# Kernel tuning notes

Hardware: AMD Instinct MI355X
Metric: run time of the kernel (lower is better)

Reference implementation:

```python
import jax, jax.numpy as jnp
import numpy as np

N_NODES = 100000

def gcn_conv(x, edge_index, W, b, n_nodes):
    # GCNConv: out = D^{-1/2} (A + I) D^{-1/2} X W + b  (self-loops added)
    src, dst = edge_index[0], edge_index[1]
    loops = jnp.arange(n_nodes, dtype=edge_index.dtype)
    src = jnp.concatenate([src, loops])
    dst = jnp.concatenate([dst, loops])
    deg = jax.ops.segment_sum(jnp.ones_like(dst, dtype=x.dtype), dst, num_segments=n_nodes)
    dinv = jnp.where(deg > 0, jax.lax.rsqrt(deg), 0.0)
    norm = dinv[src] * dinv[dst]  # [E+N]
    h = x @ W  # transform first (small d), then gather/scatter
    msgs = h[src] * norm[:, None]
    out = jax.ops.segment_sum(msgs, dst, num_segments=n_nodes)
    return out + b


def setup_inputs() -> dict:
    key = jax.random.key(0)
    k1, k2, k3, k4, k5, k6 = jax.random.split(key, 6)
    x = jax.random.normal(k1, (N_NODES, 3), dtype=jnp.float32)
    edge_index = jax.random.randint(k2, (2, 2400000), 0, N_NODES, dtype=jnp.int64)
    # Glorot-style init for GCNConv linear weights; zero bias matches PyG default
    W1 = jax.random.normal(k3, (3, 16), dtype=jnp.float32) * (1.0 / np.sqrt(3))
    b1 = jnp.zeros((16,), dtype=jnp.float32)
    W2 = jax.random.normal(k4, (16, 32), dtype=jnp.float32) * (1.0 / np.sqrt(16))
    b2 = jnp.zeros((32,), dtype=jnp.float32)
    return {"x": x, "edge_index": edge_index, "W1": W1, "b1": b1, "W2": W2, "b2": b2}


def reference(x, edge_index, W1, b1, W2, b2):
    n = x.shape[0]
    h = gcn_conv(x, edge_index, W1, b1, n)
    h = jax.nn.relu(h)
    h = gcn_conv(h, edge_index, W2, b2, n)
    # batch is all zeros in the original forward -> single-graph mean pool
    return jnp.mean(h, axis=0, keepdims=True)  # [1, 32]
```

## Files before the change

### kernel.cpp

```cpp
#include <hip/hip_runtime.h>

typedef unsigned int uint;
typedef unsigned long long ull;
typedef unsigned char uchar;


#define MAXB  256
#define CAP   16384u
#define BINB  512
#define CHUNK 4096
#define AFS   2048.0f
#define AFB   16384
#define AFM   0x1FFFFFu
#define PADN  131072

__global__ void __launch_bounds__(BINB)
bin2_kernel(const int* __restrict__ srcI, const int* __restrict__ dstI,
            uint* __restrict__ curDg, uint* __restrict__ curSg,
            uint* __restrict__ bufD, uint* __restrict__ bufS, int E) {
    __shared__ uint cntD[MAXB], scanD[MAXB], deltaD[MAXB];
    __shared__ uint cntS[MAXB], scanS[MAXB], deltaS[MAXB];
    __shared__ uint stageD[CHUNK];
    __shared__ uint stageS[CHUNK];
    __shared__ uchar stBD[CHUNK];
    __shared__ uchar stBS[CHUNK];
    const int tid = threadIdx.x;
    const int e0 = blockIdx.x * CHUNK;
    const int nE = min(CHUNK, E - e0);
    const int my0 = tid * 8;
    const int myc = max(0, min(8, nE - my0));
    if (tid < MAXB) cntD[tid] = 0u; else cntS[tid - MAXB] = 0u;

    uint d8[8], s8[8], rD[8], rS[8];
    if (myc == 8) {
        int4 ka = ((const int4*)(dstI + e0))[tid * 2];
        int4 kb = ((const int4*)(dstI + e0))[tid * 2 + 1];
        int4 oa = ((const int4*)(srcI + e0))[tid * 2];
        int4 ob = ((const int4*)(srcI + e0))[tid * 2 + 1];
        d8[0] = ka.x; d8[1] = ka.y; d8[2] = ka.z; d8[3] = ka.w;
        d8[4] = kb.x; d8[5] = kb.y; d8[6] = kb.z; d8[7] = kb.w;
        s8[0] = oa.x; s8[1] = oa.y; s8[2] = oa.z; s8[3] = oa.w;
        s8[4] = ob.x; s8[5] = ob.y; s8[6] = ob.z; s8[7] = ob.w;
    } else {
        for (int r = 0; r < myc; ++r) {
            d8[r] = (uint)dstI[e0 + my0 + r];
            s8[r] = (uint)srcI[e0 + my0 + r];
        }
    }
    __syncthreads();
    for (int r = 0; r < myc; ++r) {
        rD[r] = atomicAdd(&cntD[d8[r] >> 9], 1u);
        rS[r] = atomicAdd(&cntS[s8[r] >> 9], 1u);
    }
    __syncthreads();
    {
        const int wv = tid >> 6, lane = tid & 63;
        if (wv < 2) {
            uint* cn = wv ? cntS : cntD;
            uint* sc = wv ? scanS : scanD;
            uint v0 = cn[lane * 4], v1 = cn[lane * 4 + 1],
                 v2 = cn[lane * 4 + 2], v3 = cn[lane * 4 + 3];
            uint s1 = v0 + v1, s2 = s1 + v2, s3 = s2 + v3;
            uint tot = s3;
            for (int off = 1; off < 64; off <<= 1) {
                uint t = __shfl_up(tot, off, 64);
                if (lane >= off) tot += t;
            }
            uint basex = tot - s3;
            sc[lane * 4]     = basex + v0;
            sc[lane * 4 + 1] = basex + s1;
            sc[lane * 4 + 2] = basex + s2;
            sc[lane * 4 + 3] = basex + s3;
        }
    }
    __syncthreads();
    {
        const int half = tid >> 8;
        const int li = tid & 255;
        uint* cn = half ? cntS : cntD;
        uint* sc = half ? scanS : scanD;
        uint* cur = half ? curSg : curDg;
        uint* dl = half ? deltaS : deltaD;
        uint gbase = (uint)li * CAP + (cn[li] ? atomicAdd(&cur[li * 16], cn[li]) : 0u);
        dl[li] = gbase - (sc[li] - cn[li]);
    }
    __syncthreads();
    for (int r = 0; r < myc; ++r) {
        uint bD = d8[r] >> 9;
        uint pD = (scanD[bD] - cntD[bD]) + rD[r];
        stageD[pD] = ((d8[r] & 511u) << 17) | s8[r];
        stBD[pD] = (uchar)bD;
        uint bS = s8[r] >> 9;
        uint pS = (scanS[bS] - cntS[bS]) + rS[r];
        stageS[pS] = ((s8[r] & 511u) << 17) | d8[r];
        stBS[pS] = (uchar)bS;
    }
    __syncthreads();
#pragma unroll
    for (int r = 0; r < 8; ++r) {
        int i = r * BINB + tid;
        if (i < nE) {
            uint b = stBD[i];
            uint gp = deltaD[b] + (uint)i;
            if (gp < (b + 1u) * CAP) bufD[gp] = stageD[i];
            uint b2 = stBS[i];
            uint gp2 = deltaS[b2] + (uint)i;
            if (gp2 < (b2 + 1u) * CAP) bufS[gp2] = stageS[i];
        }
    }
}

__global__ void __launch_bounds__(1024)
degnode_kernel(const uint* __restrict__ buf, const uint* __restrict__ curD,
               const float* __restrict__ x, uint* __restrict__ degg,
               float* __restrict__ dinv, ull* __restrict__ pxd, int n) {
    __shared__ uint dg[512];
    const int tid = threadIdx.x;
    const int b = blockIdx.x;
    const uint base = (uint)b * CAP;
    const uint c = min(curD[b * 16], CAP);
    if (tid < 512) dg[tid] = 0u;
    __syncthreads();
    for (uint i0 = (uint)tid * 8u; i0 < c; i0 += 8192u) {
        uint cnt8 = min(8u, c - i0);
        uint en[8];
        if (cnt8 == 8u) {
            uint4 a = ((const uint4*)(buf + base + i0))[0];
            uint4 bb = ((const uint4*)(buf + base + i0))[1];
            en[0] = a.x; en[1] = a.y; en[2] = a.z; en[3] = a.w;
            en[4] = bb.x; en[5] = bb.y; en[6] = bb.z; en[7] = bb.w;
        } else {
            for (uint r = 0; r < cnt8; ++r) en[r] = buf[base + i0 + r];
        }
        for (uint r = 0; r < cnt8; ++r) atomicAdd(&dg[en[r] >> 17], 1u);
    }
    __syncthreads();
    if (tid < 512) {
        int node = (b << 9) + tid;
        if (node < n) {
            uint d = dg[tid];
            degg[node] = d;
            float di = rsqrtf((float)(d + 1u));
            dinv[node] = di;
            ull f0 = (ull)(uint)((int)rintf(x[3 * node] * di * AFS) + AFB);
            ull f1 = (ull)(uint)((int)rintf(x[3 * node + 1] * di * AFS) + AFB);
            ull f2 = (ull)(uint)((int)rintf(x[3 * node + 2] * di * AFS) + AFB);
            pxd[node] = f0 | (f1 << 21) | (f2 << 42);
        }
    }
}

__global__ void __launch_bounds__(1024)
aggqT_kernel(const uint* __restrict__ bufD, const uint* __restrict__ curD,
             const uint* __restrict__ bufS, const uint* __restrict__ curS,
             const uint* __restrict__ degg, const float* __restrict__ dinv,
             const ull* __restrict__ pxd, const float* __restrict__ x,
             const float* __restrict__ W1, const float* __restrict__ b1,
             const float* __restrict__ W2, const float* __restrict__ b2,
             float* __restrict__ T, uint* __restrict__ doneCtr,
             float* __restrict__ out, int n) {
    __shared__ ull acc[512];
    __shared__ float gl[512];
    __shared__ float taccs[16];
    __shared__ float tval[16];
    __shared__ int lastB;
    const int tid = threadIdx.x;
    const int b = blockIdx.x;
    const uint base = (uint)b * CAP;
    const uint cD = min(curD[b * 16], CAP);
    const uint cS = min(curS[b * 16], CAP);
    if (tid < 512) { acc[tid] = 0ull; gl[tid] = 0.0f; }
    if (tid < 16) taccs[tid] = 0.0f;
    __syncthreads();
    const int sweep = tid >> 9;
    const uint ht = (uint)(tid & 511);
    if (sweep == 0) {
        for (uint i0 = ht * 8u; i0 < cS; i0 += 4096u) {
            uint cnt8 = min(8u, cS - i0);
            uint en[8];
            if (cnt8 == 8u) {
                uint4 a = ((const uint4*)(bufS + base + i0))[0];
                uint4 bb = ((const uint4*)(bufS + base + i0))[1];
                en[0] = a.x; en[1] = a.y; en[2] = a.z; en[3] = a.w;
                en[4] = bb.x; en[5] = bb.y; en[6] = bb.z; en[7] = bb.w;
            } else {
                for (uint r = 0; r < cnt8; ++r) en[r] = bufS[base + i0 + r];
                for (uint r = cnt8; r < 8u; ++r) en[r] = en[0];
            }
            float dv[8];
#pragma unroll
            for (int r = 0; r < 8; ++r) dv[r] = dinv[en[r] & 0x1FFFFu];
#pragma unroll
            for (uint r = 0; r < 8u; ++r)
                if (r < cnt8) atomicAdd(&gl[en[r] >> 17], dv[r]);
        }
    } else {
        for (uint i0 = ht * 8u; i0 < cD; i0 += 4096u) {
            uint cnt8 = min(8u, cD - i0);
            uint en[8];
            if (cnt8 == 8u) {
                uint4 a = ((const uint4*)(bufD + base + i0))[0];
                uint4 bb = ((const uint4*)(bufD + base + i0))[1];
                en[0] = a.x; en[1] = a.y; en[2] = a.z; en[3] = a.w;
                en[4] = bb.x; en[5] = bb.y; en[6] = bb.z; en[7] = bb.w;
            } else {
                for (uint r = 0; r < cnt8; ++r) en[r] = bufD[base + i0 + r];
                for (uint r = cnt8; r < 8u; ++r) en[r] = en[0];
            }
            ull gv[8];
#pragma unroll
            for (int r = 0; r < 8; ++r) gv[r] = pxd[en[r] & 0x1FFFFu];
#pragma unroll
            for (uint r = 0; r < 8u; ++r)
                if (r < cnt8) atomicAdd(&acc[en[r] >> 17], gv[r]);
        }
    }
    __syncthreads();
    float sq[16];
#pragma unroll
    for (int k = 0; k < 16; ++k) sq[k] = 0.0f;
    if (tid < 512) {
        int node = (b << 9) + tid;
        if (node < n) {
            ull v = acc[tid];
            int ub = (int)(degg[node] * (uint)AFB);
            float di = dinv[node];
            const float isc = 1.0f / AFS;
            float av = (float)((int)(uint)(v & AFM) - ub) * isc + x[3 * node] * di;
            float bv = (float)((int)(uint)((v >> 21) & AFM) - ub) * isc + x[3 * node + 1] * di;
            float cv = (float)((int)(uint)((v >> 42) & AFM) - ub) * isc + x[3 * node + 2] * di;
            float w = gl[tid] + di;
#pragma unroll
            for (int k = 0; k < 16; ++k) {
                float h = di * (av * W1[k] + bv * W1[16 + k] + cv * W1[32 + k]) + b1[k];
                h = fmaxf(h, 0.0f);
                sq[k] = w * (di * h);
            }
        }
    }
#pragma unroll
    for (int k = 0; k < 16; ++k) {
        float v2 = sq[k];
        for (int off = 32; off > 0; off >>= 1) v2 += __shfl_down(v2, off, 64);
        if ((tid & 63) == 0) atomicAdd(&taccs[k], v2);
    }
    __syncthreads();
    if (tid < 16 && taccs[tid] != 0.0f) atomicAdd(&T[tid], taccs[tid]);
    __syncthreads();
    if (tid == 0) {
        __threadfence();
        uint t = atomicAdd(doneCtr, 1u);
        lastB = (t == (uint)(gridDim.x - 1)) ? 1 : 0;
    }
    __syncthreads();
    if (lastB) {
        if (tid < 16) tval[tid] = atomicAdd(&T[tid], 0.0f);
        __syncthreads();
        if (tid < 32) {
            float s2 = 0.0f;
#pragma unroll
            for (int k = 0; k < 16; ++k) s2 += tval[k] * W2[k * 32 + tid];
            out[tid] = b2[tid] + (1.0f / (float)n) * s2;
        }
    }
}

extern "C" void kernel_launch(void* const* d_in, const int* in_sizes, int n_in,
                              void* d_out, int out_size, void* d_ws, size_t ws_size,
                              hipStream_t stream) {
    const float* x   = (const float*)d_in[0];
    const int*   ei  = (const int*)d_in[1];
    const float* W1  = (const float*)d_in[2];
    const float* b1  = (const float*)d_in[3];
    const float* W2  = (const float*)d_in[4];
    const float* b2  = (const float*)d_in[5];
    float* out = (float*)d_out;

    const int n = in_sizes[0] / 3;
    const int E = in_sizes[1] / 2;
    const int* src = ei;
    const int* dst = ei + E;

    char* p = (char*)d_ws;
    float* T    = (float*)p;    p += 64;
    uint*  done = (uint*)p;     p += 64;
    uint*  curD = (uint*)p;     p += MAXB * 16 * 4;
    uint*  curS = (uint*)p;     p += MAXB * 16 * 4;
    size_t zbytes = (size_t)(p - (char*)d_ws);
    uint*  degg  = (uint*)p;    p += (size_t)n * 4;
    float* dinv  = (float*)p;   p += (size_t)n * 4;
    uint*  bufD  = (uint*)p;    p += (size_t)MAXB * CAP * 4;
    uint*  bufS  = (uint*)p;    p += (size_t)MAXB * CAP * 4;
    p = (char*)(((size_t)p + 31) & ~(size_t)31);
    ull*   pxd   = (ull*)p;     p += (size_t)PADN * 8;

    const int nb = (n + 511) >> 9;

    hipMemsetAsync(d_ws, 0, zbytes, stream);
    bin2_kernel<<<(E + CHUNK - 1) / CHUNK, BINB, 0, stream>>>(src, dst, curD, curS, bufD, bufS, E);
    degnode_kernel<<<nb, 1024, 0, stream>>>(bufD, curD, x, degg, dinv, pxd, n);
    aggqT_kernel<<<nb, 1024, 0, stream>>>(bufD, curD, bufS, curS, degg, dinv, pxd, x,
                                          W1, b1, W2, b2, T, done, out, n);
}
```

Before: 136.4 us.

## Fuse degree and aggregation kernels with an in-kernel grid barrier

Merges the degree-counting and node-prep kernel into the aggregation kernel. A software global barrier (atomic counter plus spin-wait) separates the phase that writes pxd/dinv from the gather phase. Each block keeps its own degree histogram in shared memory, so the degg array and one kernel launch gap go away. With 196 blocks of 1024 threads, all blocks must be co-resident or the barrier deadlocks; the guard counter only bounds the spin.

Measured after the change: 149.0 us. 1.09x slower.

```diff
diff --git a/kernel.cpp b/kernel.cpp
--- a/kernel.cpp
+++ b/kernel.cpp
@@ -110,55 +110,31 @@
     }
 }
 
+__device__ __forceinline__ void gbar(uint* ctr, uint target) {
+    __syncthreads();
+    if (threadIdx.x == 0) {
+        __threadfence();
+        atomicAdd(ctr, 1u);
+        uint guard = 0u;
+        while (__hip_atomic_load(ctr, __ATOMIC_ACQUIRE,
+                                 __HIP_MEMORY_SCOPE_AGENT) < target) {
+            __builtin_amdgcn_s_sleep(8);
+            if (++guard > 0x20000000u) break;
+        }
+    }
+    __syncthreads();
+}
+
 __global__ void __launch_bounds__(1024)
-degnode_kernel(const uint* __restrict__ buf, const uint* __restrict__ curD,
-               const float* __restrict__ x, uint* __restrict__ degg,
-               float* __restrict__ dinv, ull* __restrict__ pxd, int n) {
+degaggqT_kernel(const uint* __restrict__ bufD, const uint* __restrict__ curD,
+                const uint* __restrict__ bufS, const uint* __restrict__ curS,
+                const float* __restrict__ x,
+                const float* __restrict__ W1, const float* __restrict__ b1,
+                const float* __restrict__ W2, const float* __restrict__ b2,
+                float* __restrict__ dinv, ull* __restrict__ pxd,
+                float* __restrict__ T, uint* __restrict__ bar0,
+                uint* __restrict__ doneCtr, float* __restrict__ out, int n) {
     __shared__ uint dg[512];
-    const int tid = threadIdx.x;
-    const int b = blockIdx.x;
-    const uint base = (uint)b * CAP;
-    const uint c = min(curD[b * 16], CAP);
-    if (tid < 512) dg[tid] = 0u;
-    __syncthreads();
-    for (uint i0 = (uint)tid * 8u; i0 < c; i0 += 8192u) {
-        uint cnt8 = min(8u, c - i0);
-        uint en[8];
-        if (cnt8 == 8u) {
-            uint4 a = ((const uint4*)(buf + base + i0))[0];
-            uint4 bb = ((const uint4*)(buf + base + i0))[1];
-            en[0] = a.x; en[1] = a.y; en[2] = a.z; en[3] = a.w;
-            en[4] = bb.x; en[5] = bb.y; en[6] = bb.z; en[7] = bb.w;
-        } else {
-            for (uint r = 0; r < cnt8; ++r) en[r] = buf[base + i0 + r];
-        }
-        for (uint r = 0; r < cnt8; ++r) atomicAdd(&dg[en[r] >> 17], 1u);
-    }
-    __syncthreads();
-    if (tid < 512) {
-        int node = (b << 9) + tid;
-        if (node < n) {
-            uint d = dg[tid];
-            degg[node] = d;
-            float di = rsqrtf((float)(d + 1u));
-            dinv[node] = di;
-            ull f0 = (ull)(uint)((int)rintf(x[3 * node] * di * AFS) + AFB);
-            ull f1 = (ull)(uint)((int)rintf(x[3 * node + 1] * di * AFS) + AFB);
-            ull f2 = (ull)(uint)((int)rintf(x[3 * node + 2] * di * AFS) + AFB);
-            pxd[node] = f0 | (f1 << 21) | (f2 << 42);
-        }
-    }
-}
-
-__global__ void __launch_bounds__(1024)
-aggqT_kernel(const uint* __restrict__ bufD, const uint* __restrict__ curD,
-             const uint* __restrict__ bufS, const uint* __restrict__ curS,
-             const uint* __restrict__ degg, const float* __restrict__ dinv,
-             const ull* __restrict__ pxd, const float* __restrict__ x,
-             const float* __restrict__ W1, const float* __restrict__ b1,
-             const float* __restrict__ W2, const float* __restrict__ b2,
-             float* __restrict__ T, uint* __restrict__ doneCtr,
-             float* __restrict__ out, int n) {
     __shared__ ull acc[512];
     __shared__ float gl[512];
     __shared__ float taccs[16];
@@ -168,6 +144,36 @@
     const int b = blockIdx.x;
     const uint base = (uint)b * CAP;
     const uint cD = min(curD[b * 16], CAP);
+
+    if (tid < 512) dg[tid] = 0u;
+    __syncthreads();
+    for (uint i0 = (uint)tid * 8u; i0 < cD; i0 += 8192u) {
+        uint cnt8 = min(8u, cD - i0);
+        uint en[8];
+        if (cnt8 == 8u) {
+            uint4 a = ((const uint4*)(bufD + base + i0))[0];
+            uint4 bb = ((const uint4*)(bufD + base + i0))[1];
+            en[0] = a.x; en[1] = a.y; en[2] = a.z; en[3] = a.w;
+            en[4] = bb.x; en[5] = bb.y; en[6] = bb.z; en[7] = bb.w;
+        } else {
+            for (uint r = 0; r < cnt8; ++r) en[r] = bufD[base + i0 + r];
+        }
+        for (uint r = 0; r < cnt8; ++r) atomicAdd(&dg[en[r] >> 17], 1u);
+    }
+    __syncthreads();
+    if (tid < 512) {
+        int node = (b << 9) + tid;
+        if (node < n) {
+            float di = rsqrtf((float)(dg[tid] + 1u));
+            dinv[node] = di;
+            ull f0 = (ull)(uint)((int)rintf(x[3 * node] * di * AFS) + AFB);
+            ull f1 = (ull)(uint)((int)rintf(x[3 * node + 1] * di * AFS) + AFB);
+            ull f2 = (ull)(uint)((int)rintf(x[3 * node + 2] * di * AFS) + AFB);
+            pxd[node] = f0 | (f1 << 21) | (f2 << 42);
+        }
+    }
+    gbar(bar0, gridDim.x);
+
     const uint cS = min(curS[b * 16], CAP);
     if (tid < 512) { acc[tid] = 0ull; gl[tid] = 0.0f; }
     if (tid < 16) taccs[tid] = 0.0f;
@@ -223,8 +229,8 @@
         int node = (b << 9) + tid;
         if (node < n) {
             ull v = acc[tid];
-            int ub = (int)(degg[node] * (uint)AFB);
-            float di = dinv[node];
+            int ub = (int)(dg[tid] * (uint)AFB);
+            float di = rsqrtf((float)(dg[tid] + 1u));
             const float isc = 1.0f / AFS;
             float av = (float)((int)(uint)(v & AFM) - ub) * isc + x[3 * node] * di;
             float bv = (float)((int)(uint)((v >> 21) & AFM) - ub) * isc + x[3 * node + 1] * di;
@@ -284,10 +290,10 @@
     char* p = (char*)d_ws;
     float* T    = (float*)p;    p += 64;
     uint*  done = (uint*)p;     p += 64;
+    uint*  bar0 = (uint*)p;     p += 64;
     uint*  curD = (uint*)p;     p += MAXB * 16 * 4;
     uint*  curS = (uint*)p;     p += MAXB * 16 * 4;
     size_t zbytes = (size_t)(p - (char*)d_ws);
-    uint*  degg  = (uint*)p;    p += (size_t)n * 4;
     float* dinv  = (float*)p;   p += (size_t)n * 4;
     uint*  bufD  = (uint*)p;    p += (size_t)MAXB * CAP * 4;
     uint*  bufS  = (uint*)p;    p += (size_t)MAXB * CAP * 4;
@@ -298,7 +304,7 @@
 
     hipMemsetAsync(d_ws, 0, zbytes, stream);
     bin2_kernel<<<(E + CHUNK - 1) / CHUNK, BINB, 0, stream>>>(src, dst, curD, curS, bufD, bufS, E);
-    degnode_kernel<<<nb, 1024, 0, stream>>>(bufD, curD, x, degg, dinv, pxd, n);
-    aggqT_kernel<<<nb, 1024, 0, stream>>>(bufD, curD, bufS, curS, degg, dinv, pxd, x,
-                                          W1, b1, W2, b2, T, done, out, n);
+    degaggqT_kernel<<<nb, 1024, 0, stream>>>(bufD, curD, bufS, curS, x,
+                                             W1, b1, W2, b2, dinv, pxd,
+                                             T, bar0, done, out, n);
 }
```
